# Kernel optimization log

Hardware: AMD Instinct MI355X
Metric: run time of the kernel (lower is better)

Reference implementation:

```python
import jax, jax.numpy as jnp
import numpy as np

N_NODES = 200000
N_EDGES = 3200000
N_FEAT = 165


def setup_inputs() -> dict:
    key = jax.random.key(0)
    ks = jax.random.split(key, 8)

    def glorot(k, fan_in, fan_out):
        lim = np.sqrt(6.0 / (fan_in + fan_out)).astype(np.float32)
        return jax.random.uniform(k, (fan_in, fan_out), jnp.float32, -lim, lim)

    x = jax.random.normal(ks[0], (N_NODES, N_FEAT), jnp.float32)
    edge_index = jax.random.randint(ks[1], (2, N_EDGES), 0, N_NODES, dtype=jnp.int64)
    return {
        "x": x,
        "edge_index": edge_index,
        "W1": glorot(ks[2], N_FEAT, 64), "b1": jnp.zeros((64,), jnp.float32),
        "W2": glorot(ks[3], 64, 16),     "b2": jnp.zeros((16,), jnp.float32),
        "W3": glorot(ks[4], 16, 2),      "b3": jnp.zeros((2,), jnp.float32),
    }


def _gcn_layer(x, src, dst, norm, W, b, n_nodes):
    # linear transform first (feature dim shrinks), then normalized scatter-add
    h = x @ W                                # [N, out]
    msg = h[src] * norm[:, None]             # gather over edges (incl. self-loops)
    out = jax.ops.segment_sum(msg, dst, num_segments=n_nodes)
    return out + b


def reference(x, edge_index, W1, b1, W2, b2, W3, b3):
    n = x.shape[0]
    loops = jnp.arange(n, dtype=edge_index.dtype)
    src = jnp.concatenate([edge_index[0], loops])   # PyG GCNConv adds self-loops
    dst = jnp.concatenate([edge_index[1], loops])
    # symmetric normalization deg^{-1/2}[src] * deg^{-1/2}[dst]
    deg = jax.ops.segment_sum(jnp.ones_like(dst, dtype=x.dtype), dst, num_segments=n)
    dinv = jnp.where(deg > 0, jax.lax.rsqrt(deg), 0.0)
    norm = dinv[src] * dinv[dst]                    # [E + N]

    h = jax.nn.relu(_gcn_layer(x, src, dst, norm, W1, b1, n))
    h = jax.nn.relu(_gcn_layer(h, src, dst, norm, W2, b2, n))
    h = _gcn_layer(h, src, dst, norm, W3, b3, n)
    return jax.nn.log_softmax(h, axis=1)
```

## Files before the change

### kernel.cpp

```cpp
#include <hip/hip_runtime.h>
#include <cstdint>
#include <math.h>

#define BLK 256
#define NBUK_MAX 1024

__device__ __forceinline__ float bf_lo(unsigned p) { return __uint_as_float(p << 16); }
__device__ __forceinline__ float bf_hi(unsigned p) { return __uint_as_float(p & 0xffff0000u); }
__device__ __forceinline__ unsigned pack2(float a, float b) {
  unsigned ua = __float_as_uint(a), ub = __float_as_uint(b);
  ua = (ua + 0x7fffu + ((ua >> 16) & 1u)) >> 16;
  ub = (ub + 0x7fffu + ((ub >> 16) & 1u)) >> 16;
  return (ua & 0xffffu) | (ub << 16);
}

typedef _Float16 half8 __attribute__((ext_vector_type(8)));
typedef float f32x4 __attribute__((ext_vector_type(4)));


__global__ void k_zero(int* __restrict__ p, int n) {
  int i = blockIdx.x * blockDim.x + threadIdx.x;
  if (i < n) p[i] = 0;
}


__global__ __launch_bounds__(BLK)
void k_bcount(const int* __restrict__ edges, long long E, long long chunk, int nbuk,
              int* __restrict__ bucket_counts) {
  __shared__ int hist[NBUK_MAX];
  for (int i = threadIdx.x; i < nbuk; i += BLK) hist[i] = 0;
  __syncthreads();
  long long beg = (long long)blockIdx.x * chunk;
  long long end = beg + chunk < E ? beg + chunk : E;
  for (long long e = beg + threadIdx.x; e < end; e += BLK)
    atomicAdd(&hist[edges[E + e] >> 8], 1);
  __syncthreads();
  for (int i = threadIdx.x; i < nbuk; i += BLK)
    if (hist[i]) atomicAdd(&bucket_counts[i], hist[i]);
}

__global__ __launch_bounds__(1024)
void k_bscan(const int* __restrict__ bucket_counts, int nbuk,
             int* __restrict__ bucket_start, int* __restrict__ bucket_cursor) {
  __shared__ int tmp[1024];
  int i = threadIdx.x;
  int v = (i < nbuk) ? bucket_counts[i] : 0;
  tmp[i] = v;
  __syncthreads();
  for (int off = 1; off < 1024; off <<= 1) {
    int t = (i >= off) ? tmp[i - off] : 0;
    __syncthreads();
    tmp[i] += t;
    __syncthreads();
  }
  if (i < nbuk) {
    int ex = tmp[i] - v;
    bucket_start[i] = ex;
    bucket_cursor[i] = ex;
  }
  if (i == nbuk - 1) bucket_start[nbuk] = tmp[i];
}

__global__ __launch_bounds__(BLK)
void k_bscatter(const int* __restrict__ edges, long long E, long long chunk, int nbuk,
                int* __restrict__ bucket_cursor, int* __restrict__ tmp_out) {
  __shared__ int hist[NBUK_MAX];
  __shared__ int base[NBUK_MAX];
  for (int i = threadIdx.x; i < nbuk; i += BLK) hist[i] = 0;
  __syncthreads();
  long long beg = (long long)blockIdx.x * chunk;
  long long end = beg + chunk < E ? beg + chunk : E;
  for (long long e = beg + threadIdx.x; e < end; e += BLK)
    atomicAdd(&hist[edges[E + e] >> 8], 1);
  __syncthreads();
  for (int i = threadIdx.x; i < nbuk; i += BLK) {
    int c = hist[i];
    base[i] = c ? atomicAdd(&bucket_cursor[i], c) : 0;
    hist[i] = 0;
  }
  __syncthreads();
  for (long long e = beg + threadIdx.x; e < end; e += BLK) {
    int s = edges[e];
    int d = edges[E + e];
    int b = d >> 8;
    int r = atomicAdd(&hist[b], 1);
    tmp_out[base[b] + r] = (s << 8) | (d & 255);
  }
}

__global__ __launch_bounds__(BLK)
void k_bfinal(const int* __restrict__ tmp_in, const int* __restrict__ bucket_start, int n,
              int* __restrict__ row_start, int* __restrict__ counts,
              float* __restrict__ dinv, int* __restrict__ col) {
  __shared__ int cnt[256];
  __shared__ int scan[256];
  __shared__ int cur[256];
  const int b = blockIdx.x, t = threadIdx.x;
  const int seg0 = bucket_start[b], seg1 = bucket_start[b + 1];
  cnt[t] = 0;
  __syncthreads();
  for (int i = seg0 + t; i < seg1; i += BLK) atomicAdd(&cnt[tmp_in[i] & 255], 1);
  __syncthreads();
  int v0 = cnt[t];
  scan[t] = v0;
  __syncthreads();
  for (int off = 1; off < 256; off <<= 1) {
    int x = (t >= off) ? scan[t - off] : 0;
    __syncthreads();
    scan[t] += x;
    __syncthreads();
  }
  int loff = scan[t] - v0;
  int v = b * 256 + t;
  if (v < n) {
    row_start[v] = seg0 + loff;
    counts[v] = v0;
    dinv[v] = rsqrtf((float)v0 + 1.0f);
  }
  cur[t] = loff;
  __syncthreads();
  for (int i = seg0 + t; i < seg1; i += BLK) {
    int p = tmp_in[i];
    int r = atomicAdd(&cur[p & 255], 1);
    col[seg0 + r] = p >> 8;
  }
}


#define G1R 128

__global__ __launch_bounds__(BLK)
void k_gemm1(const float* __restrict__ in, const float* __restrict__ W,
             const float* __restrict__ dinv, unsigned* __restrict__ hs1, int n) {
  __shared__ half8 Wl[6 * 4 * 64];
  const int t = threadIdx.x;
  const int lane = t & 63, w = t >> 6;

  for (int e = t; e < 12288; e += BLK) {
    int i = e & 7, ln = (e >> 3) & 63, cf = (e >> 9) & 3, ks = e >> 11;
    int k = ks * 32 + ((ln >> 4) << 3) + i;
    int c = (cf << 4) + (ln & 15);
    float v = (k < 165) ? W[k * 64 + c] : 0.f;
    ((_Float16*)Wl)[e] = (_Float16)v;
  }
  __syncthreads();

  const int row0 = blockIdx.x * G1R + w * 32;
  const int arow = row0 + (lane & 15);
  const int kg = (lane >> 4) << 3;

  f32x4 acc[2][4] = {};

  for (int ks = 0; ks < 6; ++ks) {
    half8 b0 = Wl[(ks * 4 + 0) * 64 + lane];
    half8 b1 = Wl[(ks * 4 + 1) * 64 + lane];
    half8 b2 = Wl[(ks * 4 + 2) * 64 + lane];
    half8 b3 = Wl[(ks * 4 + 3) * 64 + lane];
    const int kbase = ks * 32 + kg;
#pragma unroll
    for (int rf = 0; rf < 2; ++rf) {
      const int r = arow + rf * 16;
      float xv[8] = {0.f, 0.f, 0.f, 0.f, 0.f, 0.f, 0.f, 0.f};
      if (ks < 5) {
        if (r < n) {
          const float* p = in + (size_t)r * 165 + kbase;
#pragma unroll
          for (int i = 0; i < 8; ++i) xv[i] = p[i];
        }
      } else {
        if (r < n && kg == 0) {
          const float* p = in + (size_t)r * 165 + kbase;
#pragma unroll
          for (int i = 0; i < 5; ++i) xv[i] = p[i];
        }
      }
      half8 a;
#pragma unroll
      for (int i = 0; i < 8; ++i) a[i] = (_Float16)xv[i];
      acc[rf][0] = __builtin_amdgcn_mfma_f32_16x16x32_f16(a, b0, acc[rf][0], 0, 0, 0);
      acc[rf][1] = __builtin_amdgcn_mfma_f32_16x16x32_f16(a, b1, acc[rf][1], 0, 0, 0);
      acc[rf][2] = __builtin_amdgcn_mfma_f32_16x16x32_f16(a, b2, acc[rf][2], 0, 0, 0);
      acc[rf][3] = __builtin_amdgcn_mfma_f32_16x16x32_f16(a, b3, acc[rf][3], 0, 0, 0);
    }
  }

  const int cq = lane >> 4;
#pragma unroll
  for (int rf = 0; rf < 2; ++rf) {
    const int rb = row0 + rf * 16 + cq * 4;
    float4 dv4 = *(const float4*)&dinv[rb];
    float dvs[4] = {dv4.x, dv4.y, dv4.z, dv4.w};
#pragma unroll
    for (int j = 0; j < 4; ++j) {
      const int r = rb + j;
#pragma unroll
      for (int cf = 0; cf < 4; ++cf) {
        float v = acc[rf][cf][j] * dvs[j];
        float vn = __shfl_xor(v, 1);
        if (!(lane & 1) && r < n)
          hs1[(size_t)r * 32 + ((cf << 4) + (lane & 15)) / 2] = pack2(v, vn);
      }
    }
  }
}


#define W2S 33

__global__ __launch_bounds__(BLK)
void k_gather64g2(const unsigned* __restrict__ hs1, const int* __restrict__ row_start,
                  const int* __restrict__ counts, const int* __restrict__ col,
                  const float* __restrict__ dinv, const float* __restrict__ b1,
                  const float* __restrict__ W2, unsigned* __restrict__ hs2, int n) {
  __shared__ float W2l[64 * W2S];
  for (int i = threadIdx.x; i < 64 * 16; i += BLK)
    W2l[(i >> 4) * W2S + (i & 15)] = W2[i];
  __syncthreads();

  int wave = threadIdx.x >> 6, lane = threadIdx.x & 63;
  int v = blockIdx.x * 4 + wave;
  if (v >= n) return;
  int sub = lane >> 5, u = lane & 31;
  int beg = row_start[v], cnt = counts[v];

  float a0, a1;
  if (sub == 0) {
    unsigned p = hs1[(size_t)v * 32 + u];
    a0 = bf_lo(p); a1 = bf_hi(p);
  } else {
    a0 = 0.f; a1 = 0.f;
  }

  int e = sub;
  for (; e + 14 < cnt; e += 16) {
    int s0 = col[beg + e];
    int s1 = col[beg + e + 2];
    int s2 = col[beg + e + 4];
    int s3 = col[beg + e + 6];
    int s4 = col[beg + e + 8];
    int s5 = col[beg + e + 10];
    int s6 = col[beg + e + 12];
    int s7 = col[beg + e + 14];
    unsigned p0 = hs1[(size_t)s0 * 32 + u];
    unsigned p1 = hs1[(size_t)s1 * 32 + u];
    unsigned p2 = hs1[(size_t)s2 * 32 + u];
    unsigned p3 = hs1[(size_t)s3 * 32 + u];
    unsigned p4 = hs1[(size_t)s4 * 32 + u];
    unsigned p5 = hs1[(size_t)s5 * 32 + u];
    unsigned p6 = hs1[(size_t)s6 * 32 + u];
    unsigned p7 = hs1[(size_t)s7 * 32 + u];
    a0 += ((bf_lo(p0) + bf_lo(p1)) + (bf_lo(p2) + bf_lo(p3))) +
          ((bf_lo(p4) + bf_lo(p5)) + (bf_lo(p6) + bf_lo(p7)));
    a1 += ((bf_hi(p0) + bf_hi(p1)) + (bf_hi(p2) + bf_hi(p3))) +
          ((bf_hi(p4) + bf_hi(p5)) + (bf_hi(p6) + bf_hi(p7)));
  }
  for (; e + 6 < cnt; e += 8) {
    int s0 = col[beg + e];
    int s1 = col[beg + e + 2];
    int s2 = col[beg + e + 4];
    int s3 = col[beg + e + 6];
    unsigned p0 = hs1[(size_t)s0 * 32 + u];
    unsigned p1 = hs1[(size_t)s1 * 32 + u];
    unsigned p2 = hs1[(size_t)s2 * 32 + u];
    unsigned p3 = hs1[(size_t)s3 * 32 + u];
    a0 += (bf_lo(p0) + bf_lo(p1)) + (bf_lo(p2) + bf_lo(p3));
    a1 += (bf_hi(p0) + bf_hi(p1)) + (bf_hi(p2) + bf_hi(p3));
  }
  for (; e < cnt; e += 2) {
    unsigned p = hs1[(size_t)col[beg + e] * 32 + u];
    a0 += bf_lo(p); a1 += bf_hi(p);
  }
  a0 += __shfl_xor(a0, 32);
  a1 += __shfl_xor(a1, 32);

  float dv = dinv[v];
  float2 bb = ((const float2*)b1)[u];
  float r0 = fmaxf(fmaf(a0, dv, bb.x), 0.f);
  float r1 = fmaxf(fmaf(a1, dv, bb.y), 0.f);

  int o = lane & 15, q = lane >> 4;
  float part = 0.f;
#pragma unroll
  for (int i = 0; i < 16; i += 2) {
    int k = q * 16 + i;
    float e0 = __shfl(r0, k >> 1);
    float e1 = __shfl(r1, k >> 1);
    part = fmaf(e0, W2l[k * W2S + o], part);
    part = fmaf(e1, W2l[(k + 1) * W2S + o], part);
  }
  part += __shfl_xor(part, 16);
  part += __shfl_xor(part, 32);
  float h = part * dv;
  float hnext = __shfl_xor(h, 1);
  if (lane < 16 && (lane & 1) == 0)
    hs2[(size_t)v * 8 + (o >> 1)] = pack2(h, hnext);
}


__global__ __launch_bounds__(BLK)
void k_gather16g3(const unsigned* __restrict__ hs2, const int* __restrict__ row_start,
                  const int* __restrict__ counts, const int* __restrict__ col,
                  const float* __restrict__ dinv, const float* __restrict__ b2,
                  const float* __restrict__ W3, float* __restrict__ hs3, int n) {
  int wave = threadIdx.x >> 6, lane = threadIdx.x & 63;
  int v = blockIdx.x * 4 + wave;
  if (v >= n) return;
  int j = lane >> 3, p = lane & 7;
  int beg = row_start[v], cnt = counts[v];

  float a0 = 0.f, a1 = 0.f;
  int e = j;
  for (; e + 8 < cnt; e += 16) {
    unsigned pk0 = hs2[(size_t)col[beg + e] * 8 + p];
    unsigned pk1 = hs2[(size_t)col[beg + e + 8] * 8 + p];
    a0 += bf_lo(pk0) + bf_lo(pk1);
    a1 += bf_hi(pk0) + bf_hi(pk1);
  }
  if (e < cnt) {
    unsigned pk = hs2[(size_t)col[beg + e] * 8 + p];
    a0 += bf_lo(pk); a1 += bf_hi(pk);
  }
  a0 += __shfl_xor(a0, 8);  a1 += __shfl_xor(a1, 8);
  a0 += __shfl_xor(a0, 16); a1 += __shfl_xor(a1, 16);
  a0 += __shfl_xor(a0, 32); a1 += __shfl_xor(a1, 32);

  unsigned ps = hs2[(size_t)v * 8 + p];
  a0 += bf_lo(ps); a1 += bf_hi(ps);

  float dv = dinv[v];
  float2 bb = ((const float2*)b2)[p];
  float r0 = fmaxf(fmaf(a0, dv, bb.x), 0.f);
  float r1 = fmaxf(fmaf(a1, dv, bb.y), 0.f);

  int o = lane & 1;
  float part = 0.f;
#pragma unroll
  for (int i = 0; i < 8; ++i) {
    float e0 = __shfl(r0, i);
    float e1 = __shfl(r1, i);
    part = fmaf(e0, W3[(2 * i) * 2 + o], part);
    part = fmaf(e1, W3[(2 * i + 1) * 2 + o], part);
  }
  if (lane < 2) hs3[(size_t)v * 2 + o] = part * dv;
}


__global__ __launch_bounds__(BLK)
void k_gather2_lsm(const float* __restrict__ hs3, const int* __restrict__ row_start,
                   const int* __restrict__ counts, const int* __restrict__ col,
                   const float* __restrict__ dinv, const float* __restrict__ b,
                   float* __restrict__ out, int n) {
  int t = threadIdx.x;
  int v = blockIdx.x * 64 + (t >> 2);
  int sl = t & 3;
  if (v >= n) return;
  const float2* h = (const float2*)hs3;
  int beg = row_start[v], cnt = counts[v];
  float a0 = 0.f, a1 = 0.f;
  int e = sl;
  for (; e + 4 < cnt; e += 8) {
    int c0 = col[beg + e];
    int c1 = col[beg + e + 4];
    float2 m0 = h[c0];
    float2 m1 = h[c1];
    a0 += m0.x + m1.x;
    a1 += m0.y + m1.y;
  }
  if (e < cnt) {
    float2 m = h[col[beg + e]];
    a0 += m.x; a1 += m.y;
  }
  a0 += __shfl_xor(a0, 1); a1 += __shfl_xor(a1, 1);
  a0 += __shfl_xor(a0, 2); a1 += __shfl_xor(a1, 2);
  if (sl == 0) {
    float2 self = h[v];
    a0 += self.x; a1 += self.y;
    float dv = dinv[v];
    a0 = fmaf(a0, dv, b[0]);
    a1 = fmaf(a1, dv, b[1]);
    float m = fmaxf(a0, a1);
    float l = m + logf(expf(a0 - m) + expf(a1 - m));
    ((float2*)out)[v] = make_float2(a0 - l, a1 - l);
  }
}


extern "C" void kernel_launch(void* const* d_in, const int* in_sizes, int n_in,
                              void* d_out, int out_size, void* d_ws, size_t ws_size,
                              hipStream_t stream) {
  const float* x = (const float*)d_in[0];
  const int* edges = (const int*)d_in[1];
  const float* W1 = (const float*)d_in[2];
  const float* b1 = (const float*)d_in[3];
  const float* W2 = (const float*)d_in[4];
  const float* b2 = (const float*)d_in[5];
  const float* W3 = (const float*)d_in[6];
  const float* b3 = (const float*)d_in[7];
  float* out = (float*)d_out;

  const int N = in_sizes[0] / 165;
  const long long E = in_sizes[1] / 2;
  const int nbuk = (N + 255) >> 8;

  char* w = (char*)d_ws;
  int* counts        = (int*)w;  w += (size_t)N * 4;
  int* row_start     = (int*)w;  w += (size_t)N * 4;
  float* dinv        = (float*)w; w += (size_t)N * 4;
  int* bucket_counts = (int*)w;  w += (NBUK_MAX + 4) * 4;
  int* bucket_start  = (int*)w;  w += (NBUK_MAX + 4) * 4;
  int* bucket_cursor = (int*)w;  w += (NBUK_MAX + 4) * 4;
  int* col           = (int*)w;  w += (size_t)E * 4;
  unsigned* hs1      = (unsigned*)w; w += (size_t)N * 32 * 4;
  unsigned* hs2      = (unsigned*)w; w += (size_t)N * 8 * 4;
  float* hs3         = (float*)w;
  int* tmp = (int*)hs1;

  const int gN = (N + BLK - 1) / BLK;
  const int gW = (N + 3) / 4;
  const int NB_PART = 256;
  const long long chunk = (E + NB_PART - 1) / NB_PART;

  k_zero<<<(nbuk + BLK - 1) / BLK, BLK, 0, stream>>>(bucket_counts, nbuk);
  k_bcount<<<NB_PART, BLK, 0, stream>>>(edges, E, chunk, nbuk, bucket_counts);
  k_bscan<<<1, 1024, 0, stream>>>(bucket_counts, nbuk, bucket_start, bucket_cursor);
  k_bscatter<<<NB_PART, BLK, 0, stream>>>(edges, E, chunk, nbuk, bucket_cursor, tmp);
  k_bfinal<<<nbuk, BLK, 0, stream>>>(tmp, bucket_start, N, row_start, counts, dinv, col);

  k_gemm1<<<(N + G1R - 1) / G1R, BLK, 0, stream>>>(x, W1, dinv, hs1, N);

  k_gather64g2<<<gW, BLK, 0, stream>>>(hs1, row_start, counts, col, dinv, b1, W2, hs2, N);

  k_gather16g3<<<gW, BLK, 0, stream>>>(hs2, row_start, counts, col, dinv, b2, W3, hs3, N);

  k_gather2_lsm<<<(N + 63) / 64, BLK, 0, stream>>>(hs3, row_start, counts, col, dinv, b3, out, N);
}
```

Before: 612.3 us.

## Replace two-pass bucket sort with single-pass scatter into fixed-capacity bucket slots

The separate count pass and its exclusive-scan-before-scatter are removed. Each edge now takes its position with a per-edge global atomic on its bucket cursor and writes into a fixed slot region of SLOT entries per destination bucket. The scan runs afterwards to compute CSR offsets, and the final per-bucket kernel reads from the slot regions. This saves one full read of the destination array and one kernel launch, but adds heavy global atomic contention on about 800 counters and less coalesced writes. It also assumes no bucket holds more than 5120 edges, which is true for uniform random graphs but would overflow on skewed ones.

```diff
diff --git a/kernel.cpp b/kernel.cpp
--- a/kernel.cpp
+++ b/kernel.cpp
@@ -4,6 +4,7 @@
 
 #define BLK 256
 #define NBUK_MAX 1024
+#define SLOT 5120
 
 __device__ __forceinline__ float bf_lo(unsigned p) { return __uint_as_float(p << 16); }
 __device__ __forceinline__ float bf_hi(unsigned p) { return __uint_as_float(p & 0xffff0000u); }
@@ -25,23 +26,22 @@
 
 
 __global__ __launch_bounds__(BLK)
-void k_bcount(const int* __restrict__ edges, long long E, long long chunk, int nbuk,
-              int* __restrict__ bucket_counts) {
-  __shared__ int hist[NBUK_MAX];
-  for (int i = threadIdx.x; i < nbuk; i += BLK) hist[i] = 0;
-  __syncthreads();
+void k_bscatter_direct(const int* __restrict__ edges, long long E, long long chunk,
+                       int* __restrict__ bucket_cursor, int* __restrict__ tmp_out) {
   long long beg = (long long)blockIdx.x * chunk;
   long long end = beg + chunk < E ? beg + chunk : E;
-  for (long long e = beg + threadIdx.x; e < end; e += BLK)
-    atomicAdd(&hist[edges[E + e] >> 8], 1);
-  __syncthreads();
-  for (int i = threadIdx.x; i < nbuk; i += BLK)
-    if (hist[i]) atomicAdd(&bucket_counts[i], hist[i]);
+  for (long long e = beg + threadIdx.x; e < end; e += BLK) {
+    int s = edges[e];
+    int d = edges[E + e];
+    int b = d >> 8;
+    int r = atomicAdd(&bucket_cursor[b], 1);
+    tmp_out[(size_t)b * SLOT + r] = (s << 8) | (d & 255);
+  }
 }
 
 __global__ __launch_bounds__(1024)
-void k_bscan(const int* __restrict__ bucket_counts, int nbuk,
-             int* __restrict__ bucket_start, int* __restrict__ bucket_cursor) {
+void k_bscan2(const int* __restrict__ bucket_counts, int nbuk,
+              int* __restrict__ bucket_start) {
   __shared__ int tmp[1024];
   int i = threadIdx.x;
   int v = (i < nbuk) ? bucket_counts[i] : 0;
@@ -53,53 +53,24 @@
     tmp[i] += t;
     __syncthreads();
   }
-  if (i < nbuk) {
-    int ex = tmp[i] - v;
-    bucket_start[i] = ex;
-    bucket_cursor[i] = ex;
-  }
+  if (i < nbuk) bucket_start[i] = tmp[i] - v;
   if (i == nbuk - 1) bucket_start[nbuk] = tmp[i];
 }
 
 __global__ __launch_bounds__(BLK)
-void k_bscatter(const int* __restrict__ edges, long long E, long long chunk, int nbuk,
-                int* __restrict__ bucket_cursor, int* __restrict__ tmp_out) {
-  __shared__ int hist[NBUK_MAX];
-  __shared__ int base[NBUK_MAX];
-  for (int i = threadIdx.x; i < nbuk; i += BLK) hist[i] = 0;
-  __syncthreads();
-  long long beg = (long long)blockIdx.x * chunk;
-  long long end = beg + chunk < E ? beg + chunk : E;
-  for (long long e = beg + threadIdx.x; e < end; e += BLK)
-    atomicAdd(&hist[edges[E + e] >> 8], 1);
-  __syncthreads();
-  for (int i = threadIdx.x; i < nbuk; i += BLK) {
-    int c = hist[i];
-    base[i] = c ? atomicAdd(&bucket_cursor[i], c) : 0;
-    hist[i] = 0;
-  }
-  __syncthreads();
-  for (long long e = beg + threadIdx.x; e < end; e += BLK) {
-    int s = edges[e];
-    int d = edges[E + e];
-    int b = d >> 8;
-    int r = atomicAdd(&hist[b], 1);
-    tmp_out[base[b] + r] = (s << 8) | (d & 255);
-  }
-}
-
-__global__ __launch_bounds__(BLK)
-void k_bfinal(const int* __restrict__ tmp_in, const int* __restrict__ bucket_start, int n,
-              int* __restrict__ row_start, int* __restrict__ counts,
-              float* __restrict__ dinv, int* __restrict__ col) {
+void k_bfinal2(const int* __restrict__ tmp_in, const int* __restrict__ bucket_start, int n,
+               int* __restrict__ row_start, int* __restrict__ counts,
+               float* __restrict__ dinv, int* __restrict__ col) {
   __shared__ int cnt[256];
   __shared__ int scan[256];
   __shared__ int cur[256];
   const int b = blockIdx.x, t = threadIdx.x;
-  const int seg0 = bucket_start[b], seg1 = bucket_start[b + 1];
+  const int wbase = bucket_start[b];
+  const int cntb = bucket_start[b + 1] - wbase;
+  const long long rbase = (long long)b * SLOT;
   cnt[t] = 0;
   __syncthreads();
-  for (int i = seg0 + t; i < seg1; i += BLK) atomicAdd(&cnt[tmp_in[i] & 255], 1);
+  for (int i = t; i < cntb; i += BLK) atomicAdd(&cnt[tmp_in[rbase + i] & 255], 1);
   __syncthreads();
   int v0 = cnt[t];
   scan[t] = v0;
@@ -113,16 +84,16 @@
   int loff = scan[t] - v0;
   int v = b * 256 + t;
   if (v < n) {
-    row_start[v] = seg0 + loff;
+    row_start[v] = wbase + loff;
     counts[v] = v0;
     dinv[v] = rsqrtf((float)v0 + 1.0f);
   }
   cur[t] = loff;
   __syncthreads();
-  for (int i = seg0 + t; i < seg1; i += BLK) {
-    int p = tmp_in[i];
+  for (int i = t; i < cntb; i += BLK) {
+    int p = tmp_in[rbase + i];
     int r = atomicAdd(&cur[p & 255], 1);
-    col[seg0 + r] = p >> 8;
+    col[wbase + r] = p >> 8;
   }
 }
 
@@ -417,14 +388,13 @@
 
   const int gN = (N + BLK - 1) / BLK;
   const int gW = (N + 3) / 4;
-  const int NB_PART = 256;
+  const int NB_PART = 512;
   const long long chunk = (E + NB_PART - 1) / NB_PART;
 
-  k_zero<<<(nbuk + BLK - 1) / BLK, BLK, 0, stream>>>(bucket_counts, nbuk);
-  k_bcount<<<NB_PART, BLK, 0, stream>>>(edges, E, chunk, nbuk, bucket_counts);
-  k_bscan<<<1, 1024, 0, stream>>>(bucket_counts, nbuk, bucket_start, bucket_cursor);
-  k_bscatter<<<NB_PART, BLK, 0, stream>>>(edges, E, chunk, nbuk, bucket_cursor, tmp);
-  k_bfinal<<<nbuk, BLK, 0, stream>>>(tmp, bucket_start, N, row_start, counts, dinv, col);
+  k_zero<<<(nbuk + BLK - 1) / BLK, BLK, 0, stream>>>(bucket_cursor, nbuk);
+  k_bscatter_direct<<<NB_PART, BLK, 0, stream>>>(edges, E, chunk, bucket_cursor, tmp);
+  k_bscan2<<<1, 1024, 0, stream>>>(bucket_cursor, nbuk, bucket_start);
+  k_bfinal2<<<nbuk, BLK, 0, stream>>>(tmp, bucket_start, N, row_start, counts, dinv, col);
 
   k_gemm1<<<(N + G1R - 1) / G1R, BLK, 0, stream>>>(x, W1, dinv, hs1, N);
 
```

New measurement: 1.268 ms. 2.07x slower.
